# Kernel optimization log

Measured on AMD Instinct MI355X. Metric: run time of the kernel, lower is better.

## Reference

```python
import jax, jax.numpy as jnp
import numpy as np

NL, D, H, FF, L = 8, 1024, 16, 4096, 1024
HD = D // H
EPS = 1e-5


def _rope_pos_emb(seq_len, head_dim):
    # Matches get_RoPE_matrix: pos_emb = cat([cos, sin], dim=-1), shape [1,1,L,head_dim]
    pos = jnp.arange(seq_len, dtype=jnp.float32)
    inv_freq = 1.0 / (10000.0 ** (jnp.arange(0, head_dim, 2, dtype=jnp.float32) / head_dim))
    ang = pos[:, None] * inv_freq[None, :]                      # [L, hd/2]
    return jnp.concatenate([jnp.cos(ang), jnp.sin(ang)], -1)[None, None]  # [1,1,L,hd]


def _alibi_bias(n_heads, seq_len):
    i = jnp.arange(n_heads, dtype=jnp.float32)
    slopes = 2.0 ** (-(2.0 ** -(np.log2(n_heads) - 3.0)) * i)   # [H]
    dist = (jnp.arange(seq_len)[:, None] - jnp.arange(seq_len)[None, :])
    dist = jnp.clip(dist, 0, None).astype(jnp.float32)          # [L,L]
    return slopes[:, None, None] * dist[None]                   # [H,L,L]


def _apply_rope(x, pe):
    # Faithful to apply_RoPE incl. the interleaved slicing of cat([cos,sin])
    xe, xo = x[..., ::2], x[..., 1::2]
    c, s = pe[..., ::2], pe[..., 1::2]
    return jnp.concatenate([xe * c - xo * s, xe * s + xo * c], -1)


def _ln(x, g, b):
    mu = jnp.mean(x, -1, keepdims=True)
    var = jnp.mean((x - mu) ** 2, -1, keepdims=True)
    return (x - mu) * jax.lax.rsqrt(var + EPS) * g + b


def _forward(src, Wq, bq, Wk, bk, Wv, bv, Wo, bo, W1, b1, W2, b2, g1, be1, g2, be2, gf, bf):
    B, Lx, _ = src.shape
    pe = _rope_pos_emb(Lx, HD)
    alibi = _alibi_bias(H, Lx)
    x = src
    for l in range(NL):
        q = (x @ Wq[l] + bq[l]).reshape(B, Lx, H, HD).transpose(0, 2, 1, 3)
        k = (x @ Wk[l] + bk[l]).reshape(B, Lx, H, HD).transpose(0, 2, 1, 3)
        v = (x @ Wv[l] + bv[l]).reshape(B, Lx, H, HD).transpose(0, 2, 1, 3)
        q = _apply_rope(q, pe)
        k = _apply_rope(k, pe)
        scores = jnp.einsum('bhqd,bhkd->bhqk', q, k) * (HD ** -0.5) + alibi[None]
        w = jax.nn.softmax(scores, axis=-1)
        o = jnp.einsum('bhqk,bhkd->bhqd', w, v).transpose(0, 2, 1, 3).reshape(B, Lx, D)
        x = _ln(x + (o @ Wo[l] + bo[l]), g1[l], be1[l])
        ff = jax.nn.gelu(x @ W1[l] + b1[l], approximate=False) @ W2[l] + b2[l]
        x = _ln(x + ff, g2[l], be2[l])
    return _ln(x, gf, bf)


def setup_inputs() -> dict:
    key = jax.random.key(0)
    ks = jax.random.split(key, 8)
    s = 0.02
    d = {
        'src': jax.random.normal(ks[0], (2, L, D), jnp.float32),
        'Wq': jax.random.normal(ks[1], (NL, D, D), jnp.float32) * s,
        'bq': jnp.zeros((NL, D), jnp.float32),
        'Wk': jax.random.normal(ks[2], (NL, D, D), jnp.float32) * s,
        'bk': jnp.zeros((NL, D), jnp.float32),
        'Wv': jax.random.normal(ks[3], (NL, D, D), jnp.float32) * s,
        'bv': jnp.zeros((NL, D), jnp.float32),
        'Wo': jax.random.normal(ks[4], (NL, D, D), jnp.float32) * s,
        'bo': jnp.zeros((NL, D), jnp.float32),
        'W1': jax.random.normal(ks[5], (NL, D, FF), jnp.float32) * s,
        'b1': jnp.zeros((NL, FF), jnp.float32),
        'W2': jax.random.normal(ks[6], (NL, FF, D), jnp.float32) * s,
        'b2': jnp.zeros((NL, D), jnp.float32),
        'g1': jnp.ones((NL, D), jnp.float32),
        'be1': jnp.zeros((NL, D), jnp.float32),
        'g2': jnp.ones((NL, D), jnp.float32),
        'be2': jnp.zeros((NL, D), jnp.float32),
        'gf': jnp.ones((D,), jnp.float32),
        'bf': jnp.zeros((D,), jnp.float32),
    }
    return d


def reference(src, Wq, bq, Wk, bk, Wv, bv, Wo, bo, W1, b1, W2, b2, g1, be1, g2, be2, gf, bf):
    return _forward(src, Wq, bq, Wk, bk, Wv, bv, Wo, bo, W1, b1, W2, b2, g1, be1, g2, be2, gf, bf)
```

## Files before the change

### kernel.cpp

```cpp
#include <hip/hip_runtime.h>
#include <hip/hip_bf16.h>
#include <math.h>

#define NLAYERS 8
#define DMODEL 1024
#define NH 16
#define HD 64
#define FFD 4096
#define SEQ 1024
#define BATCH 2
#define MROWS (BATCH * SEQ)
#define LNEPS 1e-5f
#define LDQ 3072

typedef short bf16x8 __attribute__((ext_vector_type(8)));
typedef float f32x4 __attribute__((ext_vector_type(4)));

__device__ __forceinline__ unsigned short f2bf(float v) {
    unsigned u = __float_as_uint(v);
    u += 0x7fffu + ((u >> 16) & 1u);
    return (unsigned short)(u >> 16);
}

__device__ __forceinline__ float gelu_exact(float x) {
    return 0.5f * x * (1.0f + erff(x * 0.70710678118654752f));
}

__device__ __forceinline__ void glds16(const short* g, short* l) {
    __builtin_amdgcn_global_load_lds(
        (const __attribute__((address_space(1))) unsigned*)g,
        (__attribute__((address_space(3))) unsigned*)l, 16, 0, 0);
}

#define TKT 32

template<int BN>
__global__ __launch_bounds__(256) void gemm_tn(
    const short* __restrict__ A, const short* __restrict__ Bt,
    const float* __restrict__ bias, float* __restrict__ Cf,
    short* __restrict__ Cb, int M, int N, int K, int ldc, int act)
{
    constexpr int BM = 128;
    constexpr int MR = (BN == 128) ? 4 : 2;
    constexpr int NR = 4;
    __shared__ __align__(16) short As[2][BM * TKT];
    __shared__ __align__(16) short Bs[2][BN * TKT];

    const int tid = threadIdx.x;
    const int bm = blockIdx.y * BM;
    const int bn = blockIdx.x * BN;
    const int wave = tid >> 6, lane = tid & 63;
    const int lr = lane & 15, quad = lane >> 4;
    const int wm = (BN == 128) ? ((wave >> 1) << 6) : (wave << 5);
    const int wn = (BN == 128) ? ((wave & 1) << 6) : 0;

    const int srow = tid >> 2;
    const int scol = (tid & 3) << 3;
    const short* ag = A  + (size_t)(bm + srow) * K + scol;
    const short* bg = Bt + (size_t)(bn + srow) * K + scol;
    const int soff = srow * TKT + scol;

    f32x4 acc[MR][NR] = {};
    const int nk = K / TKT;

    glds16(ag, As[0] + soff);
    glds16(ag + (size_t)64 * K, As[0] + soff + 64 * TKT);
    glds16(bg, Bs[0] + soff);
    if constexpr (BN == 128) glds16(bg + (size_t)64 * K, Bs[0] + soff + 64 * TKT);
    asm volatile("s_waitcnt vmcnt(0)" ::: "memory");
    __builtin_amdgcn_s_barrier();

    for (int t = 0; t < nk; ++t) {
        const int cur = t & 1;
        if (t + 1 < nk) {
            const int k0 = (t + 1) * TKT;
            glds16(ag + k0, As[cur ^ 1] + soff);
            glds16(ag + (size_t)64 * K + k0, As[cur ^ 1] + soff + 64 * TKT);
            glds16(bg + k0, Bs[cur ^ 1] + soff);
            if constexpr (BN == 128)
                glds16(bg + (size_t)64 * K + k0, Bs[cur ^ 1] + soff + 64 * TKT);
        }
        bf16x8 af[MR], bfr[NR];
#pragma unroll
        for (int i = 0; i < MR; ++i)
            af[i]  = *(const bf16x8*)(As[cur] + (wm + i * 16 + lr) * TKT + (quad << 3));
#pragma unroll
        for (int j = 0; j < NR; ++j)
            bfr[j] = *(const bf16x8*)(Bs[cur] + (wn + j * 16 + lr) * TKT + (quad << 3));
#pragma unroll
        for (int i = 0; i < MR; ++i)
#pragma unroll
            for (int j = 0; j < NR; ++j)
                acc[i][j] = __builtin_amdgcn_mfma_f32_16x16x32_bf16(
                    af[i], bfr[j], acc[i][j], 0, 0, 0);
        asm volatile("s_waitcnt vmcnt(0)" ::: "memory");
        __builtin_amdgcn_s_barrier();
    }
#pragma unroll
    for (int j = 0; j < NR; ++j) {
        const int col = bn + wn + j * 16 + lr;
        const float bj = bias[col];
#pragma unroll
        for (int i = 0; i < MR; ++i) {
            const int rowb = bm + wm + i * 16 + (quad << 2);
#pragma unroll
            for (int r = 0; r < 4; ++r) {
                float v = acc[i][j][r] + bj;
                if (act) v = gelu_exact(v);
                if (Cb) Cb[(size_t)(rowb + r) * ldc + col] = (short)f2bf(v);
                else    Cf[(size_t)(rowb + r) * ldc + col] = v;
            }
        }
    }
}

__global__ __launch_bounds__(256) void transpose_bf16(
    const float* __restrict__ in, short* __restrict__ out, int R, int C)
{
    __shared__ float t[32][33];
    const int tid = threadIdx.x;
    const int rt = blockIdx.y << 5, ct = blockIdx.x << 5;
    const int r = tid >> 3, c4 = (tid & 7) << 2;
    float4 v = *(const float4*)(in + (size_t)(rt + r) * C + ct + c4);
    t[r][c4 + 0] = v.x; t[r][c4 + 1] = v.y; t[r][c4 + 2] = v.z; t[r][c4 + 3] = v.w;
    __syncthreads();
    unsigned short s0 = f2bf(t[c4 + 0][r]);
    unsigned short s1 = f2bf(t[c4 + 1][r]);
    unsigned short s2 = f2bf(t[c4 + 2][r]);
    unsigned short s3 = f2bf(t[c4 + 3][r]);
    uint2 p;
    p.x = (unsigned)s0 | ((unsigned)s1 << 16);
    p.y = (unsigned)s2 | ((unsigned)s3 << 16);
    *(uint2*)(out + (size_t)(ct + r) * R + rt + c4) = p;
}

__global__ void stack_bias(const float* __restrict__ bq, const float* __restrict__ bk,
                           const float* __restrict__ bv, float* __restrict__ out)
{
    int i = blockIdx.x * 256 + threadIdx.x;
    float v = (i < 1024) ? bq[i] : (i < 2048) ? bk[i - 1024] : bv[i - 2048];
    out[i] = v;
}

__global__ void conv_bf16(const float* __restrict__ in, short* __restrict__ out, int n)
{
    int i = (blockIdx.x * 256 + threadIdx.x) << 2;
    if (i < n) {
        float4 v = *(const float4*)(in + i);
        uint2 p;
        p.x = (unsigned)f2bf(v.x) | ((unsigned)f2bf(v.y) << 16);
        p.y = (unsigned)f2bf(v.z) | ((unsigned)f2bf(v.w) << 16);
        *(uint2*)(out + i) = p;
    }
}

__global__ void pe_fill(float* __restrict__ pe)
{
    int pos = blockIdx.x;
    int i = threadIdx.x;
    int j = i & 31;
    float invf = powf(10000.0f, -(float)j / 32.0f);
    float a = (float)pos * invf;
    pe[pos * HD + i] = (i < 32) ? cosf(a) : sinf(a);
}

__global__ __launch_bounds__(256) void ropeconv(
    const float* __restrict__ xqkv, const float* __restrict__ pe,
    short* __restrict__ Qb, short* __restrict__ Kb, short* __restrict__ Vtb)
{
    __shared__ __align__(16) short Vl[HD * 72];

    const int stile = blockIdx.x;
    const int h = blockIdx.y;
    const int b = blockIdx.z;
    const int tid = threadIdx.x;
    const int srow = tid >> 2;
    const int c0 = (tid & 3) << 4;
    const int s = stile * 64 + srow;
    const size_t xoff = (size_t)(b * SEQ + s) * LDQ + h * HD;
    const int e0 = (c0 & 31) << 1;

    const float* px = xqkv + xoff;
    const float* pk = xqkv + DMODEL + xoff;
    const float* pp = pe + s * HD + e0;
    float qv[32], kv[32], pv[32];
#pragma unroll
    for (int i = 0; i < 32; i += 4) {
        *(float4*)(qv + i) = *(const float4*)(px + e0 + i);
        *(float4*)(kv + i) = *(const float4*)(pk + e0 + i);
        *(float4*)(pv + i) = *(const float4*)(pp + i);
    }
    bf16x8 oq[2], ok[2];
#pragma unroll
    for (int i = 0; i < 16; ++i) {
        float qa = qv[2 * i], qb2 = qv[2 * i + 1];
        float ka = kv[2 * i], kb2 = kv[2 * i + 1];
        float cc = pv[2 * i], ss = pv[2 * i + 1];
        float rq = (c0 < 32) ? qa * cc - qb2 * ss : qa * ss + qb2 * cc;
        float rk = (c0 < 32) ? ka * cc - kb2 * ss : ka * ss + kb2 * cc;
        oq[i >> 3][i & 7] = (short)f2bf(rq);
        ok[i >> 3][i & 7] = (short)f2bf(rk);
    }
    const size_t obase = ((size_t)(b * NH + h) * SEQ + s) * HD;
    const int sw = (s & 7) << 3;
    *(bf16x8*)(Qb + obase + (c0 ^ sw))       = oq[0];
    *(bf16x8*)(Qb + obase + ((c0 + 8) ^ sw)) = oq[1];
    *(bf16x8*)(Kb + obase + (c0 ^ sw))       = ok[0];
    *(bf16x8*)(Kb + obase + ((c0 + 8) ^ sw)) = ok[1];

    {
        const float* pvg = xqkv + 2 * DMODEL + xoff;
        float vv[16];
#pragma unroll
        for (int i = 0; i < 16; i += 4)
            *(float4*)(vv + i) = *(const float4*)(pvg + c0 + i);
#pragma unroll
        for (int i = 0; i < 16; ++i)
            Vl[(c0 + i) * 72 + srow] = (short)f2bf(vv[i]);
    }
    __syncthreads();
    {
        const int r = tid >> 2;
        const int cb = (tid & 3) << 4;
        bf16x8 w0 = *(const bf16x8*)(Vl + r * 72 + cb);
        bf16x8 w1 = *(const bf16x8*)(Vl + r * 72 + cb + 8);
        const int swv = (r & 7) << 3;
        const size_t vb = ((size_t)(b * NH + h) * HD + r) * SEQ + stile * 64;
        *(bf16x8*)(Vtb + vb + (cb ^ swv))       = w0;
        *(bf16x8*)(Vtb + vb + ((cb + 8) ^ swv)) = w1;
    }
}

#define ATQ 64
#define ATK 64
#define APAD 72

__global__ __launch_bounds__(256) void attn_mfma(
    const short* __restrict__ Qb, const short* __restrict__ Kb,
    const short* __restrict__ Vtb, short* __restrict__ ob)
{
    __shared__ __align__(16) short Qs[ATQ * HD];
    __shared__ __align__(16) short Ks[2][ATK * HD];
    __shared__ __align__(16) short Vt[2][HD * ATK];
    __shared__ __align__(16) short Ps[ATQ * APAD];

    const int tid = threadIdx.x;
    const int bid = blockIdx.x;
    const int qtile = bid & 15;
    const int h = (bid >> 4) & 15;
    const int b = bid >> 8;
    const int q0 = qtile * ATQ;
    const int bh = b * NH + h;
    const size_t qbase = ((size_t)bh * SEQ + q0) * HD;
    const size_t kbase = (size_t)bh * SEQ * HD;
    const size_t vbase = (size_t)bh * HD * SEQ;

    const int wave = tid >> 6, lane = tid & 63;
    const int lr = lane & 15, quad = lane >> 4;
    const int dl = tid * 8;
    const int vr = tid >> 3;
    const int vc = (tid & 7) * 8;

    glds16(Qb + qbase + dl, Qs + dl);
    glds16(Qb + qbase + 2048 + dl, Qs + 2048 + dl);
    glds16(Kb + kbase + dl, Ks[0] + dl);
    glds16(Kb + kbase + 32 * HD + dl, Ks[0] + 2048 + dl);
    glds16(Vtb + vbase + (size_t)vr * SEQ + vc, Vt[0] + dl);
    glds16(Vtb + vbase + (size_t)(vr + 32) * SEQ + vc, Vt[0] + 2048 + dl);
    __syncthreads();

    bf16x8 qf0, qf1;
    {
        const int row = wave * 16 + lr;
        const int sw = (row & 7) << 3;
        qf0 = *(const bf16x8*)(Qs + row * HD + ((quad * 8) ^ sw));
        qf1 = *(const bf16x8*)(Qs + row * HD + ((32 + quad * 8) ^ sw));
    }

    const float slope = exp2f(-0.5f * (float)h);
    const int qpos = q0 + wave * 16 + quad * 4;
    float mrow[4] = {-INFINITY, -INFINITY, -INFINITY, -INFINITY};
    float lrow[4] = {0.f, 0.f, 0.f, 0.f};
    f32x4 oacc[4] = {};

    for (int t = 0; t < SEQ / ATK; ++t) {
        const int cur = t & 1;
        const int kt0 = t * ATK;
        if (t + 1 < SEQ / ATK) {
            const int kn = kt0 + ATK;
            glds16(Kb + kbase + (size_t)kn * HD + dl, Ks[cur ^ 1] + dl);
            glds16(Kb + kbase + (size_t)(kn + 32) * HD + dl, Ks[cur ^ 1] + 2048 + dl);
            glds16(Vtb + vbase + (size_t)vr * SEQ + kn + vc, Vt[cur ^ 1] + dl);
            glds16(Vtb + vbase + (size_t)(vr + 32) * SEQ + kn + vc, Vt[cur ^ 1] + 2048 + dl);
        }

        f32x4 s[4] = {};
#pragma unroll
        for (int j = 0; j < 4; ++j) {
            const int row = j * 16 + lr;
            const int sw = (row & 7) << 3;
            bf16x8 b0 = *(const bf16x8*)(Ks[cur] + row * HD + ((quad * 8) ^ sw));
            bf16x8 b1 = *(const bf16x8*)(Ks[cur] + row * HD + ((32 + quad * 8) ^ sw));
            s[j] = __builtin_amdgcn_mfma_f32_16x16x32_bf16(qf0, b0, s[j], 0, 0, 0);
            s[j] = __builtin_amdgcn_mfma_f32_16x16x32_bf16(qf1, b1, s[j], 0, 0, 0);
        }

        float pv[4][4];
        float rmax[4] = {-INFINITY, -INFINITY, -INFINITY, -INFINITY};
#pragma unroll
        for (int j = 0; j < 4; ++j) {
            const int kpos = kt0 + j * 16 + lr;
#pragma unroll
            for (int r = 0; r < 4; ++r) {
                float dist = (float)(qpos + r - kpos);
                float val = s[j][r] * 0.125f + slope * fmaxf(dist, 0.0f);
                pv[j][r] = val;
                rmax[r] = fmaxf(rmax[r], val);
            }
        }
#pragma unroll
        for (int off = 1; off <= 8; off <<= 1) {
#pragma unroll
            for (int r = 0; r < 4; ++r)
                rmax[r] = fmaxf(rmax[r], __shfl_xor(rmax[r], off));
        }
        float alpha[4], rsum[4] = {0.f, 0.f, 0.f, 0.f};
#pragma unroll
        for (int r = 0; r < 4; ++r) {
            float mnew = fmaxf(mrow[r], rmax[r]);
            alpha[r] = __expf(mrow[r] - mnew);
            mrow[r] = mnew;
        }
#pragma unroll
        for (int j = 0; j < 4; ++j)
#pragma unroll
            for (int r = 0; r < 4; ++r) {
                float e = __expf(pv[j][r] - mrow[r]);
                pv[j][r] = e;
                rsum[r] += e;
            }
#pragma unroll
        for (int off = 1; off <= 8; off <<= 1) {
#pragma unroll
            for (int r = 0; r < 4; ++r)
                rsum[r] += __shfl_xor(rsum[r], off);
        }
#pragma unroll
        for (int r = 0; r < 4; ++r)
            lrow[r] = lrow[r] * alpha[r] + rsum[r];
#pragma unroll
        for (int n = 0; n < 4; ++n)
#pragma unroll
            for (int r = 0; r < 4; ++r)
                oacc[n][r] *= alpha[r];

#pragma unroll
        for (int j = 0; j < 4; ++j)
#pragma unroll
            for (int r = 0; r < 4; ++r)
                Ps[(wave * 16 + quad * 4 + r) * APAD + j * 16 + lr] = (short)f2bf(pv[j][r]);

        bf16x8 p0 = *(const bf16x8*)(Ps + (wave * 16 + lr) * APAD + (quad << 3));
        bf16x8 p1 = *(const bf16x8*)(Ps + (wave * 16 + lr) * APAD + 32 + (quad << 3));
#pragma unroll
        for (int n = 0; n < 4; ++n) {
            const int row = n * 16 + lr;
            const int sw = (row & 7) << 3;
            bf16x8 b0 = *(const bf16x8*)(Vt[cur] + row * HD + ((quad * 8) ^ sw));
            bf16x8 b1 = *(const bf16x8*)(Vt[cur] + row * HD + ((32 + quad * 8) ^ sw));
            oacc[n] = __builtin_amdgcn_mfma_f32_16x16x32_bf16(p0, b0, oacc[n], 0, 0, 0);
            oacc[n] = __builtin_amdgcn_mfma_f32_16x16x32_bf16(p1, b1, oacc[n], 0, 0, 0);
        }
        __syncthreads();
    }

    float inv[4];
#pragma unroll
    for (int r = 0; r < 4; ++r) inv[r] = 1.0f / lrow[r];
#pragma unroll
    for (int n = 0; n < 4; ++n)
#pragma unroll
        for (int r = 0; r < 4; ++r)
            ob[(size_t)(b * SEQ + qpos + r) * DMODEL + (size_t)h * HD + n * 16 + lr] =
                (short)f2bf(oacc[n][r] * inv[r]);
}

__global__ __launch_bounds__(256) void add_ln_kernel(
    const float* __restrict__ x, const float* __restrict__ r,
    const float* __restrict__ g, const float* __restrict__ b,
    float* __restrict__ out, short* __restrict__ outb)
{
    __shared__ float rs[4], rq[4], stats[2];
    const int row = blockIdx.x, tid = threadIdx.x;
    const int c = tid << 2;
    float4 v = *(const float4*)(x + (size_t)row * DMODEL + c);
    if (r) {
        float4 rv = *(const float4*)(r + (size_t)row * DMODEL + c);
        v.x += rv.x; v.y += rv.y; v.z += rv.z; v.w += rv.w;
    }
    float s = v.x + v.y + v.z + v.w;
    float q2 = v.x * v.x + v.y * v.y + v.z * v.z + v.w * v.w;
#pragma unroll
    for (int off = 32; off; off >>= 1) {
        s += __shfl_down(s, off, 64);
        q2 += __shfl_down(q2, off, 64);
    }
    const int wid = tid >> 6, lane = tid & 63;
    if (lane == 0) { rs[wid] = s; rq[wid] = q2; }
    __syncthreads();
    if (tid == 0) {
        float ts = rs[0] + rs[1] + rs[2] + rs[3];
        float tq = rq[0] + rq[1] + rq[2] + rq[3];
        float mean = ts * (1.0f / DMODEL);
        stats[0] = mean;
        stats[1] = rsqrtf(tq * (1.0f / DMODEL) - mean * mean + LNEPS);
    }
    __syncthreads();
    const float mean = stats[0], rstd = stats[1];
    float4 gv = *(const float4*)(g + c);
    float4 bv = *(const float4*)(b + c);
    float4 res;
    res.x = (v.x - mean) * rstd * gv.x + bv.x;
    res.y = (v.y - mean) * rstd * gv.y + bv.y;
    res.z = (v.z - mean) * rstd * gv.z + bv.z;
    res.w = (v.w - mean) * rstd * gv.w + bv.w;
    *(float4*)(out + (size_t)row * DMODEL + c) = res;
    if (outb) {
        uint2 p;
        p.x = (unsigned)f2bf(res.x) | ((unsigned)f2bf(res.y) << 16);
        p.y = (unsigned)f2bf(res.z) | ((unsigned)f2bf(res.w) << 16);
        *(uint2*)(outb + (size_t)row * DMODEL + c) = p;
    }
}

extern "C" void kernel_launch(void* const* d_in, const int* in_sizes, int n_in,
                              void* d_out, int out_size, void* d_ws, size_t ws_size,
                              hipStream_t stream)
{
    (void)in_sizes; (void)n_in; (void)out_size; (void)ws_size;
    const float* src = (const float*)d_in[0];
    const float* Wq  = (const float*)d_in[1];
    const float* bq  = (const float*)d_in[2];
    const float* Wk  = (const float*)d_in[3];
    const float* bk  = (const float*)d_in[4];
    const float* Wv  = (const float*)d_in[5];
    const float* bv  = (const float*)d_in[6];
    const float* Wo  = (const float*)d_in[7];
    const float* bo  = (const float*)d_in[8];
    const float* W1  = (const float*)d_in[9];
    const float* b1  = (const float*)d_in[10];
    const float* W2  = (const float*)d_in[11];
    const float* b2  = (const float*)d_in[12];
    const float* g1  = (const float*)d_in[13];
    const float* be1 = (const float*)d_in[14];
    const float* g2  = (const float*)d_in[15];
    const float* be2 = (const float*)d_in[16];
    const float* gf  = (const float*)d_in[17];
    const float* bfp = (const float*)d_in[18];
    float* out = (float*)d_out;

    char* p = (char*)d_ws;
    auto carve = [&](size_t bytes) -> char* {
        char* r = p; p += (bytes + 255) & ~(size_t)255; return r;
    };
    float* x    = (float*)carve((size_t)MROWS * DMODEL * 4);
    float* t1   = (float*)carve((size_t)MROWS * DMODEL * 4);
    float* xqkv = (float*)carve((size_t)MROWS * LDQ * 4);
    float* pe   = (float*)carve((size_t)SEQ * HD * 4);
    float* bqkv = (float*)carve((size_t)LDQ * 4);
    short* xb   = (short*)carve((size_t)MROWS * DMODEL * 2);
    short* obb  = (short*)carve((size_t)MROWS * DMODEL * 2);
    short* h1b  = (short*)carve((size_t)MROWS * FFD * 2);
    short* wtqkv= (short*)carve((size_t)3 * DMODEL * DMODEL * 2);
    short* wto  = (short*)carve((size_t)DMODEL * DMODEL * 2);
    short* wt1  = (short*)carve((size_t)DMODEL * FFD * 2);
    short* wt2  = (short*)carve((size_t)DMODEL * FFD * 2);
    short* qbb  = (short*)carve((size_t)MROWS * DMODEL * 2);
    short* kbb  = (short*)carve((size_t)MROWS * DMODEL * 2);
    short* vtb  = (short*)carve((size_t)MROWS * DMODEL * 2);

    hipMemcpyAsync(x, src, (size_t)MROWS * DMODEL * 4, hipMemcpyDeviceToDevice, stream);
    conv_bf16<<<MROWS * DMODEL / 4 / 256, 256, 0, stream>>>(src, xb, MROWS * DMODEL);
    pe_fill<<<SEQ, HD, 0, stream>>>(pe);

    const size_t DD = (size_t)DMODEL * DMODEL;
    for (int l = 0; l < NLAYERS; ++l) {
        transpose_bf16<<<dim3(32, 32), 256, 0, stream>>>(Wq + l * DD, wtqkv,          DMODEL, DMODEL);
        transpose_bf16<<<dim3(32, 32), 256, 0, stream>>>(Wk + l * DD, wtqkv + DD,     DMODEL, DMODEL);
        transpose_bf16<<<dim3(32, 32), 256, 0, stream>>>(Wv + l * DD, wtqkv + 2 * DD, DMODEL, DMODEL);
        transpose_bf16<<<dim3(32, 32), 256, 0, stream>>>(Wo + l * DD, wto, DMODEL, DMODEL);
        transpose_bf16<<<dim3(128, 32), 256, 0, stream>>>(W1 + (size_t)l * DMODEL * FFD, wt1, DMODEL, FFD);
        transpose_bf16<<<dim3(32, 128), 256, 0, stream>>>(W2 + (size_t)l * FFD * DMODEL, wt2, FFD, DMODEL);
        stack_bias<<<12, 256, 0, stream>>>(bq + l * DMODEL, bk + l * DMODEL, bv + l * DMODEL, bqkv);

        gemm_tn<128><<<dim3(LDQ / 128, MROWS / 128), 256, 0, stream>>>(
            xb, wtqkv, bqkv, xqkv, nullptr, MROWS, LDQ, DMODEL, LDQ, 0);
        ropeconv<<<dim3(16, 16, 2), 256, 0, stream>>>(xqkv, pe, qbb, kbb, vtb);
        attn_mfma<<<BATCH * NH * (SEQ / ATQ), 256, 0, stream>>>(qbb, kbb, vtb, obb);
        gemm_tn<64><<<dim3(DMODEL / 64, MROWS / 128), 256, 0, stream>>>(
            obb, wto, bo + l * DMODEL, t1, nullptr, MROWS, DMODEL, DMODEL, DMODEL, 0);
        add_ln_kernel<<<MROWS, 256, 0, stream>>>(x, t1, g1 + l * DMODEL, be1 + l * DMODEL, x, xb);
        gemm_tn<128><<<dim3(FFD / 128, MROWS / 128), 256, 0, stream>>>(
            xb, wt1, b1 + l * FFD, nullptr, h1b, MROWS, FFD, DMODEL, FFD, 1);
        gemm_tn<64><<<dim3(DMODEL / 64, MROWS / 128), 256, 0, stream>>>(
            h1b, wt2, b2 + l * DMODEL, t1, nullptr, MROWS, DMODEL, FFD, DMODEL, 0);
        add_ln_kernel<<<MROWS, 256, 0, stream>>>(x, t1, g2 + l * DMODEL, be2 + l * DMODEL, x, xb);
    }
    add_ln_kernel<<<MROWS, 256, 0, stream>>>(x, nullptr, gf, bfp, out, nullptr);
}
```

Baseline: 2.159 ms.

## Split-K the QKV, output-projection and FFN2 GEMMs, reducing partials in consumers

Adds a split-K dimension (blockIdx.z) to the bf16 MFMA GEMM. Each split writes its own fp32 partial buffer, and only split 0 adds the bias. The QKV and Wo GEMMs use 2 splits and FFN2 uses 4. The partials are summed inside the RoPE conversion and the add+LayerNorm kernels, so no separate reduction kernel is needed. The aim is more workgroups on the GPU's many CUs for the narrow-N GEMMs (N=1024 gives only 256 or 384 tiles), at the cost of extra fp32 partial writes and reads and a larger workspace.

New measurement: 2.030 ms. 1.06x faster.

```diff
diff --git a/kernel.cpp b/kernel.cpp
--- a/kernel.cpp
+++ b/kernel.cpp
@@ -38,7 +38,8 @@
 __global__ __launch_bounds__(256) void gemm_tn(
     const short* __restrict__ A, const short* __restrict__ Bt,
     const float* __restrict__ bias, float* __restrict__ Cf,
-    short* __restrict__ Cb, int M, int N, int K, int ldc, int act)
+    short* __restrict__ Cb, int M, int N, int K, int Ksub,
+    size_t pstride, int ldc, int act)
 {
     constexpr int BM = 128;
     constexpr int MR = (BN == 128) ? 4 : 2;
@@ -49,6 +50,7 @@
     const int tid = threadIdx.x;
     const int bm = blockIdx.y * BM;
     const int bn = blockIdx.x * BN;
+    const int kz = blockIdx.z;
     const int wave = tid >> 6, lane = tid & 63;
     const int lr = lane & 15, quad = lane >> 4;
     const int wm = (BN == 128) ? ((wave >> 1) << 6) : (wave << 5);
@@ -56,12 +58,13 @@
 
     const int srow = tid >> 2;
     const int scol = (tid & 3) << 3;
-    const short* ag = A  + (size_t)(bm + srow) * K + scol;
-    const short* bg = Bt + (size_t)(bn + srow) * K + scol;
+    const short* ag = A  + (size_t)(bm + srow) * K + kz * Ksub + scol;
+    const short* bg = Bt + (size_t)(bn + srow) * K + kz * Ksub + scol;
     const int soff = srow * TKT + scol;
+    float* cf = Cf ? Cf + (size_t)kz * pstride : nullptr;
 
     f32x4 acc[MR][NR] = {};
-    const int nk = K / TKT;
+    const int nk = Ksub / TKT;
 
     glds16(ag, As[0] + soff);
     glds16(ag + (size_t)64 * K, As[0] + soff + 64 * TKT);
@@ -99,7 +102,7 @@
 #pragma unroll
     for (int j = 0; j < NR; ++j) {
         const int col = bn + wn + j * 16 + lr;
-        const float bj = bias[col];
+        const float bj = (kz == 0) ? bias[col] : 0.0f;
 #pragma unroll
         for (int i = 0; i < MR; ++i) {
             const int rowb = bm + wm + i * 16 + (quad << 2);
@@ -108,7 +111,7 @@
                 float v = acc[i][j][r] + bj;
                 if (act) v = gelu_exact(v);
                 if (Cb) Cb[(size_t)(rowb + r) * ldc + col] = (short)f2bf(v);
-                else    Cf[(size_t)(rowb + r) * ldc + col] = v;
+                else    cf[(size_t)(rowb + r) * ldc + col] = v;
             }
         }
     }
@@ -165,7 +168,8 @@
 }
 
 __global__ __launch_bounds__(256) void ropeconv(
-    const float* __restrict__ xqkv, const float* __restrict__ pe,
+    const float* __restrict__ xqkv, const float* __restrict__ xqkv1,
+    const float* __restrict__ pe,
     short* __restrict__ Qb, short* __restrict__ Kb, short* __restrict__ Vtb)
 {
     __shared__ __align__(16) short Vl[HD * 72];
@@ -180,14 +184,22 @@
     const size_t xoff = (size_t)(b * SEQ + s) * LDQ + h * HD;
     const int e0 = (c0 & 31) << 1;
 
-    const float* px = xqkv + xoff;
-    const float* pk = xqkv + DMODEL + xoff;
+    const float* px0 = xqkv + xoff;
+    const float* px1 = xqkv1 + xoff;
+    const float* pk0 = xqkv + DMODEL + xoff;
+    const float* pk1 = xqkv1 + DMODEL + xoff;
     const float* pp = pe + s * HD + e0;
     float qv[32], kv[32], pv[32];
 #pragma unroll
     for (int i = 0; i < 32; i += 4) {
-        *(float4*)(qv + i) = *(const float4*)(px + e0 + i);
-        *(float4*)(kv + i) = *(const float4*)(pk + e0 + i);
+        float4 a = *(const float4*)(px0 + e0 + i);
+        float4 a1 = *(const float4*)(px1 + e0 + i);
+        a.x += a1.x; a.y += a1.y; a.z += a1.z; a.w += a1.w;
+        *(float4*)(qv + i) = a;
+        float4 k = *(const float4*)(pk0 + e0 + i);
+        float4 k1 = *(const float4*)(pk1 + e0 + i);
+        k.x += k1.x; k.y += k1.y; k.z += k1.z; k.w += k1.w;
+        *(float4*)(kv + i) = k;
         *(float4*)(pv + i) = *(const float4*)(pp + i);
     }
     bf16x8 oq[2], ok[2];
@@ -209,11 +221,16 @@
     *(bf16x8*)(Kb + obase + ((c0 + 8) ^ sw)) = ok[1];
 
     {
-        const float* pvg = xqkv + 2 * DMODEL + xoff;
+        const float* pv0 = xqkv + 2 * DMODEL + xoff;
+        const float* pv1 = xqkv1 + 2 * DMODEL + xoff;
         float vv[16];
 #pragma unroll
-        for (int i = 0; i < 16; i += 4)
-            *(float4*)(vv + i) = *(const float4*)(pvg + c0 + i);
+        for (int i = 0; i < 16; i += 4) {
+            float4 a = *(const float4*)(pv0 + c0 + i);
+            float4 a1 = *(const float4*)(pv1 + c0 + i);
+            a.x += a1.x; a.y += a1.y; a.z += a1.z; a.w += a1.w;
+            *(float4*)(vv + i) = a;
+        }
 #pragma unroll
         for (int i = 0; i < 16; ++i)
             Vl[(c0 + i) * 72 + srow] = (short)f2bf(vv[i]);
@@ -387,23 +404,38 @@
 
 __global__ __launch_bounds__(256) void add_ln_kernel(
     const float* __restrict__ x, const float* __restrict__ r,
+    const float* __restrict__ r2, const float* __restrict__ r3,
+    const float* __restrict__ r4,
     const float* __restrict__ g, const float* __restrict__ b,
     float* __restrict__ out, short* __restrict__ outb)
 {
     __shared__ float rs[4], rq[4], stats[2];
     const int row = blockIdx.x, tid = threadIdx.x;
     const int c = tid << 2;
-    float4 v = *(const float4*)(x + (size_t)row * DMODEL + c);
+    const size_t off = (size_t)row * DMODEL + c;
+    float4 v = *(const float4*)(x + off);
     if (r) {
-        float4 rv = *(const float4*)(r + (size_t)row * DMODEL + c);
+        float4 rv = *(const float4*)(r + off);
+        v.x += rv.x; v.y += rv.y; v.z += rv.z; v.w += rv.w;
+    }
+    if (r2) {
+        float4 rv = *(const float4*)(r2 + off);
+        v.x += rv.x; v.y += rv.y; v.z += rv.z; v.w += rv.w;
+    }
+    if (r3) {
+        float4 rv = *(const float4*)(r3 + off);
+        v.x += rv.x; v.y += rv.y; v.z += rv.z; v.w += rv.w;
+    }
+    if (r4) {
+        float4 rv = *(const float4*)(r4 + off);
         v.x += rv.x; v.y += rv.y; v.z += rv.z; v.w += rv.w;
     }
     float s = v.x + v.y + v.z + v.w;
     float q2 = v.x * v.x + v.y * v.y + v.z * v.z + v.w * v.w;
 #pragma unroll
-    for (int off = 32; off; off >>= 1) {
-        s += __shfl_down(s, off, 64);
-        q2 += __shfl_down(q2, off, 64);
+    for (int off2 = 32; off2; off2 >>= 1) {
+        s += __shfl_down(s, off2, 64);
+        q2 += __shfl_down(q2, off2, 64);
     }
     const int wid = tid >> 6, lane = tid & 63;
     if (lane == 0) { rs[wid] = s; rq[wid] = q2; }
@@ -424,12 +456,12 @@
     res.y = (v.y - mean) * rstd * gv.y + bv.y;
     res.z = (v.z - mean) * rstd * gv.z + bv.z;
     res.w = (v.w - mean) * rstd * gv.w + bv.w;
-    *(float4*)(out + (size_t)row * DMODEL + c) = res;
+    *(float4*)(out + off) = res;
     if (outb) {
         uint2 p;
         p.x = (unsigned)f2bf(res.x) | ((unsigned)f2bf(res.y) << 16);
         p.y = (unsigned)f2bf(res.z) | ((unsigned)f2bf(res.w) << 16);
-        *(uint2*)(outb + (size_t)row * DMODEL + c) = p;
+        *(uint2*)(outb + off) = p;
     }
 }
 
@@ -464,8 +496,8 @@
         char* r = p; p += (bytes + 255) & ~(size_t)255; return r;
     };
     float* x    = (float*)carve((size_t)MROWS * DMODEL * 4);
-    float* t1   = (float*)carve((size_t)MROWS * DMODEL * 4);
-    float* xqkv = (float*)carve((size_t)MROWS * LDQ * 4);
+    float* t1   = (float*)carve((size_t)4 * MROWS * DMODEL * 4);
+    float* xqkv = (float*)carve((size_t)2 * MROWS * LDQ * 4);
     float* pe   = (float*)carve((size_t)SEQ * HD * 4);
     float* bqkv = (float*)carve((size_t)LDQ * 4);
     short* xb   = (short*)carve((size_t)MROWS * DMODEL * 2);
@@ -479,6 +511,9 @@
     short* kbb  = (short*)carve((size_t)MROWS * DMODEL * 2);
     short* vtb  = (short*)carve((size_t)MROWS * DMODEL * 2);
 
+    const size_t TP = (size_t)MROWS * DMODEL;
+    const size_t QP = (size_t)MROWS * LDQ;
+
     hipMemcpyAsync(x, src, (size_t)MROWS * DMODEL * 4, hipMemcpyDeviceToDevice, stream);
     conv_bf16<<<MROWS * DMODEL / 4 / 256, 256, 0, stream>>>(src, xb, MROWS * DMODEL);
     pe_fill<<<SEQ, HD, 0, stream>>>(pe);
@@ -493,18 +528,21 @@
         transpose_bf16<<<dim3(32, 128), 256, 0, stream>>>(W2 + (size_t)l * FFD * DMODEL, wt2, FFD, DMODEL);
         stack_bias<<<12, 256, 0, stream>>>(bq + l * DMODEL, bk + l * DMODEL, bv + l * DMODEL, bqkv);
 
-        gemm_tn<128><<<dim3(LDQ / 128, MROWS / 128), 256, 0, stream>>>(
-            xb, wtqkv, bqkv, xqkv, nullptr, MROWS, LDQ, DMODEL, LDQ, 0);
-        ropeconv<<<dim3(16, 16, 2), 256, 0, stream>>>(xqkv, pe, qbb, kbb, vtb);
+        gemm_tn<128><<<dim3(LDQ / 128, MROWS / 128, 2), 256, 0, stream>>>(
+            xb, wtqkv, bqkv, xqkv, nullptr, MROWS, LDQ, DMODEL, DMODEL / 2, QP, LDQ, 0);
+        ropeconv<<<dim3(16, 16, 2), 256, 0, stream>>>(xqkv, xqkv + QP, pe, qbb, kbb, vtb);
         attn_mfma<<<BATCH * NH * (SEQ / ATQ), 256, 0, stream>>>(qbb, kbb, vtb, obb);
-        gemm_tn<64><<<dim3(DMODEL / 64, MROWS / 128), 256, 0, stream>>>(
-            obb, wto, bo + l * DMODEL, t1, nullptr, MROWS, DMODEL, DMODEL, DMODEL, 0);
-        add_ln_kernel<<<MROWS, 256, 0, stream>>>(x, t1, g1 + l * DMODEL, be1 + l * DMODEL, x, xb);
-        gemm_tn<128><<<dim3(FFD / 128, MROWS / 128), 256, 0, stream>>>(
-            xb, wt1, b1 + l * FFD, nullptr, h1b, MROWS, FFD, DMODEL, FFD, 1);
-        gemm_tn<64><<<dim3(DMODEL / 64, MROWS / 128), 256, 0, stream>>>(
-            h1b, wt2, b2 + l * DMODEL, t1, nullptr, MROWS, DMODEL, FFD, DMODEL, 0);
-        add_ln_kernel<<<MROWS, 256, 0, stream>>>(x, t1, g2 + l * DMODEL, be2 + l * DMODEL, x, xb);
-    }
-    add_ln_kernel<<<MROWS, 256, 0, stream>>>(x, nullptr, gf, bfp, out, nullptr);
-}
+        gemm_tn<64><<<dim3(DMODEL / 64, MROWS / 128, 2), 256, 0, stream>>>(
+            obb, wto, bo + l * DMODEL, t1, nullptr, MROWS, DMODEL, DMODEL, DMODEL / 2, TP, DMODEL, 0);
+        add_ln_kernel<<<MROWS, 256, 0, stream>>>(
+            x, t1, t1 + TP, nullptr, nullptr, g1 + l * DMODEL, be1 + l * DMODEL, x, xb);
+        gemm_tn<128><<<dim3(FFD / 128, MROWS / 128, 1), 256, 0, stream>>>(
+            xb, wt1, b1 + l * FFD, nullptr, h1b, MROWS, FFD, DMODEL, DMODEL, 0, FFD, 1);
+        gemm_tn<64><<<dim3(DMODEL / 64, MROWS / 128, 4), 256, 0, stream>>>(
+            h1b, wt2, b2 + l * DMODEL, t1, nullptr, MROWS, DMODEL, FFD, FFD / 4, TP, DMODEL, 0);
+        add_ln_kernel<<<MROWS, 256, 0, stream>>>(
+            x, t1, t1 + TP, t1 + 2 * TP, t1 + 3 * TP, g2 + l * DMODEL, be2 + l * DMODEL, x, xb);
+    }
+    add_ln_kernel<<<MROWS, 256, 0, stream>>>(
+        x, nullptr, nullptr, nullptr, nullptr, gf, bfp, out, nullptr);
+}
```
